# Kernel optimization log

Hardware: AMD Instinct MI355X
Metric: run time of the kernel (lower is better)

Reference implementation:

```python
import jax, jax.numpy as jnp
import numpy as np

EPS = 1e-6

def _rmsnorm(x, scale):
    # RMSNorm over last axis (TPNorm pre-norm)
    var = jnp.mean(jnp.square(x), axis=-1, keepdims=True)
    return x * jax.lax.rsqrt(var + EPS) * scale


def setup_inputs() -> dict:
    key = jax.random.key(0)
    ks = jax.random.split(key, 6)
    B, S, D, H, Dh = 2, 2048, 1024, 16, 64
    x = jax.random.normal(ks[0], (B, S, D), dtype=jnp.float32)
    norm_scale = jnp.ones((D,), dtype=jnp.float32)
    # lecun_normal-like scaling: std = 1/sqrt(fan_in)
    wq = jax.random.normal(ks[1], (D, H, Dh), dtype=jnp.float32) / np.sqrt(D)
    wk = jax.random.normal(ks[2], (D, H, Dh), dtype=jnp.float32) / np.sqrt(D)
    wv = jax.random.normal(ks[3], (D, H, Dh), dtype=jnp.float32) / np.sqrt(D)
    w_out = jax.random.normal(ks[4], (H, Dh, D), dtype=jnp.float32) / np.sqrt(H * Dh)
    b_out = jnp.zeros((D,), dtype=jnp.float32)
    return {"x": x, "norm_scale": norm_scale, "wq": wq, "wk": wk, "wv": wv,
            "w_out": w_out, "b_out": b_out}


def reference(x, norm_scale, wq, wk, wv, w_out, b_out):
    dtype = x.dtype
    softmax_dtype = jnp.float32
    h = _rmsnorm(x, norm_scale)                                  # [B,S,D]
    q = jnp.einsum('bsd,dhe->bshe', h, wq)                       # [B,S,H,Dh]
    k = jnp.einsum('bsd,dhe->bshe', h, wk)
    v = jnp.einsum('bsd,dhe->bshe', h, wv)
    head_dim = q.shape[-1]
    scale = head_dim ** (-0.5)
    q = (q * scale).astype(softmax_dtype)
    kf = k.astype(softmax_dtype)
    weights = jnp.einsum('bqhd,bkhd->bhqk', q, kf)               # [B,H,S,S] fp32
    weights = jax.nn.softmax(weights, axis=-1).astype(dtype)
    new_vals = jnp.einsum('bhqk,bkhd->bqhd', weights, v).astype(dtype)
    out = jnp.einsum('bqhe,hed->bqd', new_vals, w_out) + b_out   # [B,S,D]
    return out
```

## Files before the change

kernel.cpp:

```cpp
#include <hip/hip_runtime.h>

typedef unsigned short u16;
typedef unsigned int   u32;
typedef __attribute__((ext_vector_type(8))) short bf16x8;
typedef __attribute__((ext_vector_type(4))) float f32x4;

#define SEQ 2048
#define DIM 1024
#define NH  16
#define DH  64
#define NROW 4096

static __device__ __forceinline__ float bf2f(u16 v){
  u32 u = ((u32)v) << 16; float f; __builtin_memcpy(&f, &u, 4); return f;
}
static __device__ __forceinline__ u16 f2bf(float f){
  u32 u; __builtin_memcpy(&u, &f, 4);
  u32 r = (u + 0x7fffu + ((u >> 16) & 1u)) >> 16;
  return (u16)r;
}
static __device__ __forceinline__ u32 pack2bf(float a, float b){
  u32 ua, ub; __builtin_memcpy(&ua, &a, 4); __builtin_memcpy(&ub, &b, 4);
  return ((ua + 0x8000u) >> 16) | ((ub + 0x8000u) & 0xFFFF0000u);
}
static __device__ __forceinline__ u32 cvt_pk_bf16(float a, float b){
  u32 r;
  asm("v_cvt_pk_bf16_f32 %0, %1, %2" : "=v"(r) : "v"(a), "v"(b));
  return r;
}

#define GLD_LDS(gp, lp) \
  __builtin_amdgcn_global_load_lds( \
      (const __attribute__((address_space(1))) void*)(gp), \
      (__attribute__((address_space(3))) void*)(lp), 16, 0, 0)

__global__ __launch_bounds__(256) void k_rmsnorm(const float* __restrict__ x,
                                                 const float* __restrict__ sc,
                                                 u16* __restrict__ h){
  int row = blockIdx.x, t = threadIdx.x;
  float4 v = ((const float4*)(x + (size_t)row * DIM))[t];
  float ss = v.x*v.x + v.y*v.y + v.z*v.z + v.w*v.w;
  #pragma unroll
  for (int d = 32; d; d >>= 1) ss += __shfl_down(ss, d, 64);
  __shared__ float red[4];
  if ((t & 63) == 0) red[t >> 6] = ss;
  __syncthreads();
  float tot = red[0] + red[1] + red[2] + red[3];
  float rms = rsqrtf(tot * (1.0f / DIM) + 1e-6f);
  float4 s4 = ((const float4*)sc)[t];
  u16 ov[4];
  ov[0] = f2bf(v.x * rms * s4.x);
  ov[1] = f2bf(v.y * rms * s4.y);
  ov[2] = f2bf(v.z * rms * s4.z);
  ov[3] = f2bf(v.w * rms * s4.w);
  ((uint2*)(h + (size_t)row * DIM))[t] = *(uint2*)ov;
}

__global__ __launch_bounds__(256) void k_wtrans(const float* __restrict__ in0,
                                                const float* __restrict__ in1,
                                                const float* __restrict__ in2,
                                                u16* __restrict__ outT){
  __shared__ u16 tile[64][68];
  int t = threadIdx.x;
  int c0 = blockIdx.x * 64;
  int r0 = blockIdx.y * 64;
  int z = blockIdx.z;
  const float* in = (z == 0) ? in0 : ((z == 1) ? in1 : in2);
  u16* out = outT + (size_t)z * (1u << 20);
  #pragma unroll
  for (int i = 0; i < 4; i++){
    int idx = t + 256 * i;
    int r = idx >> 4, c4 = (idx & 15) * 4;
    float4 v = *(const float4*)&in[(size_t)(r0 + r) * 1024 + c0 + c4];
    u16 pk[4] = {f2bf(v.x), f2bf(v.y), f2bf(v.z), f2bf(v.w)};
    *(uint2*)&tile[r][c4] = *(uint2*)pk;
  }
  __syncthreads();
  #pragma unroll
  for (int i = 0; i < 2; i++){
    int c = t + 256 * i;
    int n = c >> 3, koff = (c & 7) * 8;
    alignas(16) u16 vals[8];
    #pragma unroll
    for (int j = 0; j < 8; j++) vals[j] = tile[koff + j][n];
    *(uint4*)&out[(size_t)(c0 + n) * 1024 + r0 + koff] = *(uint4*)vals;
  }
}

__global__ __launch_bounds__(256) void k_gemm(const u16* __restrict__ A,
                                              const u16* __restrict__ B0,
                                              const u16* __restrict__ B1,
                                              const u16* __restrict__ B2,
                                              void* __restrict__ C0,
                                              void* __restrict__ C1,
                                              void* __restrict__ C2,
                                              const float* __restrict__ bias,
                                              int qkv){
  __shared__ u16 Al[2][128][32];
  __shared__ u16 Bl[2][128][32];
  int t = threadIdx.x, lane = t & 63, w = t >> 6;
  int wm = w & 1, wn = w >> 1;
  int mrow = lane & 15, quad = lane >> 4;
  int m0 = blockIdx.x * 128, n0 = blockIdx.y * 128;
  int z = blockIdx.z;
  const u16* Bt = (z == 0) ? B0 : ((z == 1) ? B1 : B2);

  int r0s = (t * 16) >> 6, off0 = ((t * 16) & 63) >> 1;
  int r1s = r0s + 64;

  const u16* Ap0 = &A [(size_t)(m0 + r0s) * 1024 + off0];
  const u16* Ap1 = &A [(size_t)(m0 + r1s) * 1024 + off0];
  const u16* Bp0 = &Bt[(size_t)(n0 + r0s) * 1024 + off0];
  const u16* Bp1 = &Bt[(size_t)(n0 + r1s) * 1024 + off0];

  f32x4 acc[4][4];
  #pragma unroll
  for (int ms = 0; ms < 4; ms++)
    #pragma unroll
    for (int ns = 0; ns < 4; ns++) acc[ms][ns] = (f32x4){0.f, 0.f, 0.f, 0.f};

  GLD_LDS(Ap0, &Al[0][r0s][off0]);
  GLD_LDS(Ap1, &Al[0][r1s][off0]);
  GLD_LDS(Bp0, &Bl[0][r0s][off0]);
  GLD_LDS(Bp1, &Bl[0][r1s][off0]);
  __syncthreads();

  for (int kt = 0; kt < 32; kt++){
    int cur = kt & 1;
    if (kt < 31){
      int K1 = (kt + 1) * 32;
      GLD_LDS(Ap0 + K1, &Al[cur ^ 1][r0s][off0]);
      GLD_LDS(Ap1 + K1, &Al[cur ^ 1][r1s][off0]);
      GLD_LDS(Bp0 + K1, &Bl[cur ^ 1][r0s][off0]);
      GLD_LDS(Bp1 + K1, &Bl[cur ^ 1][r1s][off0]);
    }
    bf16x8 af[4], bfr[4];
    #pragma unroll
    for (int ms = 0; ms < 4; ms++)
      af[ms] = *(const bf16x8*)&Al[cur][wm * 64 + ms * 16 + mrow][quad * 8];
    #pragma unroll
    for (int ns = 0; ns < 4; ns++)
      bfr[ns] = *(const bf16x8*)&Bl[cur][wn * 64 + ns * 16 + mrow][quad * 8];
    #pragma unroll
    for (int ms = 0; ms < 4; ms++)
      #pragma unroll
      for (int ns = 0; ns < 4; ns++)
        acc[ms][ns] = __builtin_amdgcn_mfma_f32_16x16x32_bf16(af[ms], bfr[ns], acc[ms][ns], 0, 0, 0);
    __syncthreads();
  }

  float qscale = (qkv && z == 0) ? 0.180336880111112f : 1.0f;
  bool  vmode  = (qkv && z == 2);
  void* C = (z == 0) ? C0 : ((z == 1) ? C1 : C2);

  #pragma unroll
  for (int ms = 0; ms < 4; ms++){
    #pragma unroll
    for (int ns = 0; ns < 4; ns++){
      int col = n0 + wn * 64 + ns * 16 + mrow;
      int rbase = m0 + wm * 64 + ms * 16 + quad * 4;
      if (vmode){
        int b = rbase >> 11, sl = rbase & 2047;
        int hh = col >> 6, e = col & 63;
        uint2 pk = { pack2bf(acc[ms][ns][0], acc[ms][ns][1]),
                     pack2bf(acc[ms][ns][2], acc[ms][ns][3]) };
        *(uint2*)&((u16*)C)[(size_t)((b * NH + hh) * DH + e) * SEQ + sl] = pk;
      } else if (qkv){
        #pragma unroll
        for (int r = 0; r < 4; r++)
          ((u16*)C)[(size_t)(rbase + r) * 1024 + col] = f2bf(acc[ms][ns][r] * qscale);
      } else {
        float bv = bias ? bias[col] : 0.f;
        #pragma unroll
        for (int r = 0; r < 4; r++)
          ((float*)C)[(size_t)(rbase + r) * 1024 + col] = acc[ms][ns][r] + bv;
      }
    }
  }
}

__global__ __launch_bounds__(512) void k_attn(const u16* q,
                                              const u16* __restrict__ k,
                                              const u16* __restrict__ vt,
                                              u16* nv){
  __shared__ u16 Kl[2][64][64];
  __shared__ u16 Vl[2][64][64];
  int t = threadIdx.x, lane = t & 63, w = t >> 6;
  int mrow = lane & 15, quad = lane >> 4;
  int s0 = blockIdx.x * 128;
  int bh = blockIdx.y; int b = bh >> 4, hh = bh & 15;

  const u16* qrow = q + (size_t)((b * SEQ + s0 + w * 16 + mrow) * NH + hh) * DH;
  bf16x8 bq0 = *(const bf16x8*)(qrow + quad * 8);
  bf16x8 bq1 = *(const bf16x8*)(qrow + 32 + quad * 8);

  int rw  = t >> 3;
  int fst = (rw & 3) | (((t >> 6) & 1) << 2);
  int lc  = (t & 7) ^ fst;
  const u16* kp = k  + ((size_t)b * SEQ + rw) * (NH * DH) + hh * DH + lc * 8;
  const u16* vp = vt + ((size_t)bh * DH + rw) * SEQ + lc * 8;

  int row0 = ((mrow >> 2) << 3) | (mrow & 3);
  int cK = (quad ^ ((mrow & 3) | (((mrow >> 2) & 1) << 2))) << 4;
  int cV = (quad ^ ((mrow & 3) | (((mrow >> 3) & 1) << 2))) << 4;

  f32x4 o[4];
  #pragma unroll
  for (int g = 0; g < 4; g++) o[g] = (f32x4){0.f, 0.f, 0.f, 0.f};
  f32x4 accl = (f32x4){0.f, 0.f, 0.f, 0.f};
  bf16x8 onesf;
  #pragma unroll
  for (int j = 0; j < 8; j++) onesf[j] = (short)0x3F80;

  GLD_LDS(kp, &Kl[0][0][0] + (t << 3));
  GLD_LDS(vp, &Vl[0][0][0] + (t << 3));
  kp += 64 * NH * DH; vp += 64;
  __syncthreads();

  for (int kt = 0; kt < 32; kt++){
    int cur = kt & 1;
    if (kt < 31){
      GLD_LDS(kp, &Kl[cur ^ 1][0][0] + (t << 3));
      GLD_LDS(vp, &Vl[cur ^ 1][0][0] + (t << 3));
      kp += 64 * NH * DH; vp += 64;
    }

    const char* Kb = (const char*)Kl[cur];
    f32x4 sT[4];
    #pragma unroll
    for (int g = 0; g < 4; g++){
      int rg = row0 + ((g & 1) << 2) + ((g >> 1) << 5);
      const char* rp = Kb + rg * 128;
      bf16x8 a0 = *(const bf16x8*)(rp + cK);
      bf16x8 a1 = *(const bf16x8*)(rp + (cK ^ 64));
      f32x4 zz = (f32x4){0.f, 0.f, 0.f, 0.f};
      zz = __builtin_amdgcn_mfma_f32_16x16x32_bf16(a0, bq0, zz, 0, 0, 0);
      zz = __builtin_amdgcn_mfma_f32_16x16x32_bf16(a1, bq1, zz, 0, 0, 0);
      sT[g] = zz;
    }

    u32 wd[8];
    #pragma unroll
    for (int g = 0; g < 4; g++){
      float e0 = exp2f(sT[g][0]), e1 = exp2f(sT[g][1]);
      float e2 = exp2f(sT[g][2]), e3 = exp2f(sT[g][3]);
      wd[g * 2]     = cvt_pk_bf16(e0, e1);
      wd[g * 2 + 1] = cvt_pk_bf16(e2, e3);
    }
    union { u32 u[4]; bf16x8 v; } U0, U1;
    U0.u[0] = wd[0]; U0.u[1] = wd[1]; U0.u[2] = wd[2]; U0.u[3] = wd[3];
    U1.u[0] = wd[4]; U1.u[1] = wd[5]; U1.u[2] = wd[6]; U1.u[3] = wd[7];
    bf16x8 pb0 = U0.v, pb1 = U1.v;

    accl = __builtin_amdgcn_mfma_f32_16x16x32_bf16(onesf, pb0, accl, 0, 0, 0);
    accl = __builtin_amdgcn_mfma_f32_16x16x32_bf16(onesf, pb1, accl, 0, 0, 0);

    const char* Vb = (const char*)Vl[cur];
    #pragma unroll
    for (int ge = 0; ge < 4; ge++){
      const char* rp = Vb + (ge * 16 + mrow) * 128;
      bf16x8 v0 = *(const bf16x8*)(rp + cV);
      bf16x8 v1 = *(const bf16x8*)(rp + (cV ^ 64));
      o[ge] = __builtin_amdgcn_mfma_f32_16x16x32_bf16(v0, pb0, o[ge], 0, 0, 0);
      o[ge] = __builtin_amdgcn_mfma_f32_16x16x32_bf16(v1, pb1, o[ge], 0, 0, 0);
    }

    __syncthreads();
  }

  float rl = 1.0f / accl[0];
  u16* orow = nv + (size_t)((b * SEQ + s0 + w * 16 + mrow) * NH + hh) * DH;
  #pragma unroll
  for (int ge = 0; ge < 4; ge++){
    uint2 pk = { cvt_pk_bf16(o[ge][0] * rl, o[ge][1] * rl),
                 cvt_pk_bf16(o[ge][2] * rl, o[ge][3] * rl) };
    *(uint2*)&orow[ge * 16 + quad * 4] = pk;
  }
}

extern "C" void kernel_launch(void* const* d_in, const int* in_sizes, int n_in,
                              void* d_out, int out_size, void* d_ws, size_t ws_size,
                              hipStream_t stream){
  const float* x   = (const float*)d_in[0];
  const float* nsc = (const float*)d_in[1];
  const float* wq  = (const float*)d_in[2];
  const float* wk  = (const float*)d_in[3];
  const float* wv  = (const float*)d_in[4];
  const float* wo  = (const float*)d_in[5];
  const float* bo  = (const float*)d_in[6];
  char* ws = (char*)d_ws;
  const size_t MB = (size_t)1 << 20;

  u16* qb  = (u16*)(ws);
  u16* kb  = (u16*)(ws + 8  * MB);
  u16* vtb = (u16*)(ws + 16 * MB);
  u16* h   = (u16*)d_out;
  u16* wT  = (u16*)((char*)d_out + 8 * MB);
  u16* wqT = wT;
  u16* wkT = wT + (1u << 20);
  u16* wvT = wT + (2u << 20);
  u16* woT = kb;

  k_rmsnorm<<<NROW, 256, 0, stream>>>(x, nsc, h);
  k_wtrans<<<dim3(16, 16, 3), 256, 0, stream>>>(wq, wk, wv, wT);
  k_gemm<<<dim3(32, 8, 3), 256, 0, stream>>>(h, wqT, wkT, wvT, qb, kb, vtb, nullptr, 1);
  k_attn<<<dim3(16, 32, 1), 512, 0, stream>>>(qb, kb, vtb, qb);
  k_wtrans<<<dim3(16, 16, 1), 256, 0, stream>>>(wo, wo, wo, woT);
  k_gemm<<<dim3(32, 8, 1), 256, 0, stream>>>(qb, woT, woT, woT, d_out, d_out, d_out, bo, 0);
}
```

Before: 215.1 us.

## Triple-buffer GEMM and attention loads with vmcnt waits and XCD-aware block remap

Both the GEMM and attention kernels move from double to triple LDS buffering. Each iteration now waits with explicit s_waitcnt vmcnt plus a single barrier instead of two __syncthreads, which keeps two tiles of global-to-LDS loads in flight. The grids are flattened to 1D and block ids are remapped so that consecutive tiles land on the same XCD, to improve L2 reuse. The attention kernel also raises wave priority around its MFMA sections. The cost is more LDS per block, which may reduce occupancy, and the hand-counted vmcnt values must match the number of outstanding loads.

```diff
diff --git a/kernel.cpp b/kernel.cpp
--- a/kernel.cpp
+++ b/kernel.cpp
@@ -11,9 +11,6 @@
 #define DH  64
 #define NROW 4096
 
-static __device__ __forceinline__ float bf2f(u16 v){
-  u32 u = ((u32)v) << 16; float f; __builtin_memcpy(&f, &u, 4); return f;
-}
 static __device__ __forceinline__ u16 f2bf(float f){
   u32 u; __builtin_memcpy(&u, &f, 4);
   u32 r = (u + 0x7fffu + ((u >> 16) & 1u)) >> 16;
@@ -33,6 +30,9 @@
   __builtin_amdgcn_global_load_lds( \
       (const __attribute__((address_space(1))) void*)(gp), \
       (__attribute__((address_space(3))) void*)(lp), 16, 0, 0)
+
+#define WAIT_VM(N) asm volatile("s_waitcnt vmcnt(" #N ")" ::: "memory")
+#define CFENCE()   asm volatile("" ::: "memory")
 
 __global__ __launch_bounds__(256) void k_rmsnorm(const float* __restrict__ x,
                                                  const float* __restrict__ sc,
@@ -96,13 +96,20 @@
                                               void* __restrict__ C2,
                                               const float* __restrict__ bias,
                                               int qkv){
-  __shared__ u16 Al[2][128][32];
-  __shared__ u16 Bl[2][128][32];
+  __shared__ u16 Al[3][128][32];
+  __shared__ u16 Bl[3][128][32];
   int t = threadIdx.x, lane = t & 63, w = t >> 6;
   int wm = w & 1, wn = w >> 1;
   int mrow = lane & 15, quad = lane >> 4;
-  int m0 = blockIdx.x * 128, n0 = blockIdx.y * 128;
-  int z = blockIdx.z;
+
+  int nwgs = qkv ? 768 : 256;
+  int cpx = nwgs >> 3;
+  int id = blockIdx.x;
+  int wg = (id & 7) * cpx + (id >> 3);
+  int z = wg >> 8;
+  int rem = wg & 255;
+  int m0 = (rem >> 3) << 7;
+  int n0 = (rem & 7) << 7;
   const u16* Bt = (z == 0) ? B0 : ((z == 1) ? B1 : B2);
 
   int r0s = (t * 16) >> 6, off0 = ((t * 16) & 63) >> 1;
@@ -119,20 +126,26 @@
     #pragma unroll
     for (int ns = 0; ns < 4; ns++) acc[ms][ns] = (f32x4){0.f, 0.f, 0.f, 0.f};
 
-  GLD_LDS(Ap0, &Al[0][r0s][off0]);
-  GLD_LDS(Ap1, &Al[0][r1s][off0]);
-  GLD_LDS(Bp0, &Bl[0][r0s][off0]);
-  GLD_LDS(Bp1, &Bl[0][r1s][off0]);
-  __syncthreads();
-
+  GLD_LDS(Ap0,      &Al[0][r0s][off0]);
+  GLD_LDS(Ap1,      &Al[0][r1s][off0]);
+  GLD_LDS(Bp0,      &Bl[0][r0s][off0]);
+  GLD_LDS(Bp1,      &Bl[0][r1s][off0]);
+  GLD_LDS(Ap0 + 32, &Al[1][r0s][off0]);
+  GLD_LDS(Ap1 + 32, &Al[1][r1s][off0]);
+  GLD_LDS(Bp0 + 32, &Bl[1][r0s][off0]);
+  GLD_LDS(Bp1 + 32, &Bl[1][r1s][off0]);
+
+  int cur = 0, pf = 2;
   for (int kt = 0; kt < 32; kt++){
-    int cur = kt & 1;
-    if (kt < 31){
-      int K1 = (kt + 1) * 32;
-      GLD_LDS(Ap0 + K1, &Al[cur ^ 1][r0s][off0]);
-      GLD_LDS(Ap1 + K1, &Al[cur ^ 1][r1s][off0]);
-      GLD_LDS(Bp0 + K1, &Bl[cur ^ 1][r0s][off0]);
-      GLD_LDS(Bp1 + K1, &Bl[cur ^ 1][r1s][off0]);
+    if (kt < 31) WAIT_VM(4); else WAIT_VM(0);
+    __builtin_amdgcn_s_barrier();
+    CFENCE();
+    if (kt < 30){
+      int K2 = (kt + 2) * 32;
+      GLD_LDS(Ap0 + K2, &Al[pf][r0s][off0]);
+      GLD_LDS(Ap1 + K2, &Al[pf][r1s][off0]);
+      GLD_LDS(Bp0 + K2, &Bl[pf][r0s][off0]);
+      GLD_LDS(Bp1 + K2, &Bl[pf][r1s][off0]);
     }
     bf16x8 af[4], bfr[4];
     #pragma unroll
@@ -146,7 +159,8 @@
       #pragma unroll
       for (int ns = 0; ns < 4; ns++)
         acc[ms][ns] = __builtin_amdgcn_mfma_f32_16x16x32_bf16(af[ms], bfr[ns], acc[ms][ns], 0, 0, 0);
-    __syncthreads();
+    cur = (cur == 2) ? 0 : cur + 1;
+    pf  = (pf  == 2) ? 0 : pf  + 1;
   }
 
   float qscale = (qkv && z == 0) ? 0.180336880111112f : 1.0f;
@@ -183,12 +197,14 @@
                                               const u16* __restrict__ k,
                                               const u16* __restrict__ vt,
                                               u16* nv){
-  __shared__ u16 Kl[2][64][64];
-  __shared__ u16 Vl[2][64][64];
+  __shared__ u16 Kl[3][64][64];
+  __shared__ u16 Vl[3][64][64];
   int t = threadIdx.x, lane = t & 63, w = t >> 6;
   int mrow = lane & 15, quad = lane >> 4;
-  int s0 = blockIdx.x * 128;
-  int bh = blockIdx.y; int b = bh >> 4, hh = bh & 15;
+  int id = blockIdx.x;
+  int wg = (id & 7) * 64 + (id >> 3);
+  int s0 = (wg & 15) * 128;
+  int bh = wg >> 4; int b = bh >> 4, hh = bh & 15;
 
   const u16* qrow = q + (size_t)((b * SEQ + s0 + w * 16 + mrow) * NH + hh) * DH;
   bf16x8 bq0 = *(const bf16x8*)(qrow + quad * 8);
@@ -212,21 +228,27 @@
   #pragma unroll
   for (int j = 0; j < 8; j++) onesf[j] = (short)0x3F80;
 
-  GLD_LDS(kp, &Kl[0][0][0] + (t << 3));
-  GLD_LDS(vp, &Vl[0][0][0] + (t << 3));
+  GLD_LDS(kp, (u16*)Kl[0] + (t << 3));
+  GLD_LDS(vp, (u16*)Vl[0] + (t << 3));
   kp += 64 * NH * DH; vp += 64;
-  __syncthreads();
-
+  GLD_LDS(kp, (u16*)Kl[1] + (t << 3));
+  GLD_LDS(vp, (u16*)Vl[1] + (t << 3));
+  kp += 64 * NH * DH; vp += 64;
+
+  int cur = 0, pf = 2;
   for (int kt = 0; kt < 32; kt++){
-    int cur = kt & 1;
-    if (kt < 31){
-      GLD_LDS(kp, &Kl[cur ^ 1][0][0] + (t << 3));
-      GLD_LDS(vp, &Vl[cur ^ 1][0][0] + (t << 3));
+    if (kt < 31) WAIT_VM(2); else WAIT_VM(0);
+    __builtin_amdgcn_s_barrier();
+    CFENCE();
+    if (kt < 30){
+      GLD_LDS(kp, (u16*)Kl[pf] + (t << 3));
+      GLD_LDS(vp, (u16*)Vl[pf] + (t << 3));
       kp += 64 * NH * DH; vp += 64;
     }
 
     const char* Kb = (const char*)Kl[cur];
     f32x4 sT[4];
+    __builtin_amdgcn_s_setprio(1);
     #pragma unroll
     for (int g = 0; g < 4; g++){
       int rg = row0 + ((g & 1) << 2) + ((g >> 1) << 5);
@@ -238,6 +260,7 @@
       zz = __builtin_amdgcn_mfma_f32_16x16x32_bf16(a1, bq1, zz, 0, 0, 0);
       sT[g] = zz;
     }
+    __builtin_amdgcn_s_setprio(0);
 
     u32 wd[8];
     #pragma unroll
@@ -252,6 +275,7 @@
     U1.u[0] = wd[4]; U1.u[1] = wd[5]; U1.u[2] = wd[6]; U1.u[3] = wd[7];
     bf16x8 pb0 = U0.v, pb1 = U1.v;
 
+    __builtin_amdgcn_s_setprio(1);
     accl = __builtin_amdgcn_mfma_f32_16x16x32_bf16(onesf, pb0, accl, 0, 0, 0);
     accl = __builtin_amdgcn_mfma_f32_16x16x32_bf16(onesf, pb1, accl, 0, 0, 0);
 
@@ -264,8 +288,10 @@
       o[ge] = __builtin_amdgcn_mfma_f32_16x16x32_bf16(v0, pb0, o[ge], 0, 0, 0);
       o[ge] = __builtin_amdgcn_mfma_f32_16x16x32_bf16(v1, pb1, o[ge], 0, 0, 0);
     }
-
-    __syncthreads();
+    __builtin_amdgcn_s_setprio(0);
+
+    cur = (cur == 2) ? 0 : cur + 1;
+    pf  = (pf  == 2) ? 0 : pf  + 1;
   }
 
   float rl = 1.0f / accl[0];
@@ -303,8 +329,8 @@
 
   k_rmsnorm<<<NROW, 256, 0, stream>>>(x, nsc, h);
   k_wtrans<<<dim3(16, 16, 3), 256, 0, stream>>>(wq, wk, wv, wT);
-  k_gemm<<<dim3(32, 8, 3), 256, 0, stream>>>(h, wqT, wkT, wvT, qb, kb, vtb, nullptr, 1);
-  k_attn<<<dim3(16, 32, 1), 512, 0, stream>>>(qb, kb, vtb, qb);
+  k_gemm<<<dim3(768), 256, 0, stream>>>(h, wqT, wkT, wvT, qb, kb, vtb, nullptr, 1);
+  k_attn<<<dim3(512), 512, 0, stream>>>(qb, kb, vtb, qb);
   k_wtrans<<<dim3(16, 16, 1), 256, 0, stream>>>(wo, wo, wo, woT);
-  k_gemm<<<dim3(32, 8, 1), 256, 0, stream>>>(qb, woT, woT, woT, d_out, d_out, d_out, bo, 0);
-}
+  k_gemm<<<dim3(256), 256, 0, stream>>>(qb, woT, woT, woT, d_out, d_out, d_out, bo, 0);
+}
```

After: 210.6 us. -2.1%, faster.
